# Kernel optimization log

Measured on AMD Instinct MI355X. Metric: run time of the kernel, lower is better.

Reference implementation:

```python
import jax, jax.numpy as jnp
import numpy as np

D = 512        # embed_dim
H = 2048       # expert hidden (4*D)
E = 8          # num_experts
TOPK = 2       # num_experts_per_tok


def setup_inputs() -> dict:
    key = jax.random.key(0)
    ks = jax.random.split(key, 5)
    s = 0.02
    x = jax.random.normal(ks[0], (4, 8192, D), dtype=jnp.float32)
    gate_w = jax.random.normal(ks[1], (D, E), dtype=jnp.float32) * s
    W1 = jax.random.normal(ks[2], (E, D, H), dtype=jnp.float32) * s
    W3 = jax.random.normal(ks[3], (E, D, H), dtype=jnp.float32) * s
    W2 = jax.random.normal(ks[4], (E, H, D), dtype=jnp.float32) * s
    return {"x": x, "gate_w": gate_w, "W1": W1, "W2": W2, "W3": W3}


def reference(x, gate_w, W1, W2, W3):
    B, S, _ = x.shape
    xt = x.reshape(-1, D)                      # [T, D]
    T = xt.shape[0]
    gate_logits = xt @ gate_w                  # [T, E]
    w, idx = jax.lax.top_k(gate_logits, TOPK)  # [T, k]
    w = jax.nn.softmax(w, axis=1).astype(xt.dtype)
    # combine weights: comb[t, e] = routing weight of expert e for token t (0 if unselected)
    comb = jnp.zeros((T, E), dtype=xt.dtype).at[jnp.arange(T)[:, None], idx].add(w)
    out = jnp.zeros_like(xt)
    for e in range(E):
        h = jax.nn.silu(xt @ W1[e]) * (xt @ W3[e])   # [T, H]
        out = out + (h @ W2[e]) * comb[:, e:e + 1]
    return out.reshape(B, S, D)
```

## Files before the change

### kernel.cpp

```cpp
#include <hip/hip_runtime.h>
#include <stdint.h>

#define D_DIM 512
#define H_DIM 2048
#define E_NUM 8
#define TOPK_N 2

typedef __attribute__((ext_vector_type(8))) short bf16x8;
typedef __attribute__((ext_vector_type(4))) float f32x4;

#define GLOAD_LDS16(gsrc, ldst)                                                     \
    __builtin_amdgcn_global_load_lds(                                               \
        (const __attribute__((address_space(1))) void*)(gsrc),                      \
        (__attribute__((address_space(3))) void*)(ldst), 16, 0, 0)

static __device__ __forceinline__ unsigned short f2bf(float f) {
    unsigned u = __float_as_uint(f);
    unsigned r = (u + 0x7fffu + ((u >> 16) & 1u)) >> 16;
    return (unsigned short)r;
}

__global__ void init_kernel(int* list_token, float* list_w, unsigned short* zrow, int cap) {
    int id = blockIdx.x * blockDim.x + threadIdx.x;
    if (id < cap) { list_token[id] = -1; list_w[id] = 0.f; }
    if (id < D_DIM) zrow[id] = 0;
}

__global__ void gwt_kernel(const float* __restrict__ gw, float* __restrict__ gwT) {
    int id = blockIdx.x * blockDim.x + threadIdx.x;
    int e = id >> 9, d = id & 511;
    gwT[id] = gw[d * E_NUM + e];
}

__global__ void gate_cvt_kernel(const float* __restrict__ x, const float* __restrict__ gwT,
                                unsigned short* __restrict__ xb,
                                int* __restrict__ ridx, float* __restrict__ rw, int T) {
    int wave = threadIdx.x >> 6;
    int lane = threadIdx.x & 63;
    int t = blockIdx.x * 4 + wave;
    if (t >= T) return;
    const float* xr = x + (size_t)t * D_DIM + lane * 8;
    float4 a = *(const float4*)xr;
    float4 b = *(const float4*)(xr + 4);
    union { unsigned short s[8]; uint4 v; } o;
    o.s[0] = f2bf(a.x); o.s[1] = f2bf(a.y); o.s[2] = f2bf(a.z); o.s[3] = f2bf(a.w);
    o.s[4] = f2bf(b.x); o.s[5] = f2bf(b.y); o.s[6] = f2bf(b.z); o.s[7] = f2bf(b.w);
    *(uint4*)(xb + (size_t)t * D_DIM + lane * 8) = o.v;
    float acc[8];
#pragma unroll
    for (int e = 0; e < 8; ++e) {
        const float* g = gwT + e * D_DIM + lane * 8;
        float4 g0 = *(const float4*)g;
        float4 g1 = *(const float4*)(g + 4);
        acc[e] = a.x * g0.x + a.y * g0.y + a.z * g0.z + a.w * g0.w
               + b.x * g1.x + b.y * g1.y + b.z * g1.z + b.w * g1.w;
    }
#pragma unroll
    for (int off = 32; off > 0; off >>= 1) {
#pragma unroll
        for (int e = 0; e < 8; ++e) acc[e] += __shfl_xor(acc[e], off, 64);
    }
    if (lane == 0) {
        int e0 = 0; float l0 = acc[0];
#pragma unroll
        for (int e = 1; e < 8; ++e) if (acc[e] > l0) { l0 = acc[e]; e0 = e; }
        int e1 = -1; float l1 = -1e30f;
#pragma unroll
        for (int e = 0; e < 8; ++e) if (e != e0 && acc[e] > l1) { l1 = acc[e]; e1 = e; }
        float w0 = 1.f / (1.f + expf(l1 - l0));
        ridx[t * 2] = e0; ridx[t * 2 + 1] = e1;
        rw[t * 2] = w0;  rw[t * 2 + 1] = 1.f - w0;
    }
}

__global__ void tconv_kernel(const float* __restrict__ in, unsigned short* __restrict__ out,
                             int R, int C) {
    __shared__ float tile[32][33];
    int e = blockIdx.z;
    const float* src = in + (size_t)e * R * C;
    unsigned short* dst = out + (size_t)e * R * C;
    int c = blockIdx.x * 32 + threadIdx.x;
#pragma unroll
    for (int i = 0; i < 4; ++i) {
        int r = blockIdx.y * 32 + threadIdx.y + i * 8;
        tile[threadIdx.y + i * 8][threadIdx.x] = src[(size_t)r * C + c];
    }
    __syncthreads();
    int r2 = blockIdx.y * 32 + threadIdx.x;
#pragma unroll
    for (int i = 0; i < 4; ++i) {
        int c2 = blockIdx.x * 32 + threadIdx.y + i * 8;
        dst[(size_t)c2 * R + r2] = f2bf(tile[threadIdx.x][threadIdx.y + i * 8]);
    }
}

__global__ void hist_kernel(const int* __restrict__ ridx, int* __restrict__ partial, int npairs) {
    __shared__ int cnt[E_NUM];
    if (threadIdx.x < E_NUM) cnt[threadIdx.x] = 0;
    __syncthreads();
    for (int i = blockIdx.x * blockDim.x + threadIdx.x; i < npairs; i += gridDim.x * blockDim.x)
        atomicAdd(&cnt[ridx[i]], 1);
    __syncthreads();
    if (threadIdx.x < E_NUM) partial[blockIdx.x * E_NUM + threadIdx.x] = cnt[threadIdx.x];
}

__global__ void scan_kernel(const int* __restrict__ partial, int* __restrict__ seg,
                            int* __restrict__ block_base) {
    __shared__ int sp[64 * E_NUM];
    __shared__ int segl[E_NUM + 1];
    int tid = threadIdx.x;
    if (tid < 64 * E_NUM) sp[tid] = partial[tid];
    __syncthreads();
    if (tid == 0) {
        int off = 0;
        for (int e = 0; e < E_NUM; ++e) {
            segl[e] = off;
            int c = 0;
            for (int b = 0; b < 64; ++b) c += sp[b * E_NUM + e];
            off += (c + 127) & ~127;
        }
        segl[E_NUM] = off;
    }
    __syncthreads();
    if (tid < E_NUM) {
        int run = segl[tid];
        for (int b = 0; b < 64; ++b) { block_base[b * E_NUM + tid] = run; run += sp[b * E_NUM + tid]; }
        seg[tid] = segl[tid];
        if (tid == 0) seg[E_NUM] = segl[E_NUM];
    }
}

__global__ void scatter_kernel(const int* __restrict__ ridx, const float* __restrict__ rw,
                               const int* __restrict__ block_base,
                               int* __restrict__ list_token, float* __restrict__ list_w, int npairs) {
    __shared__ int base[E_NUM];
    __shared__ int cnt[E_NUM];
    if (threadIdx.x < E_NUM) { base[threadIdx.x] = block_base[blockIdx.x * E_NUM + threadIdx.x]; cnt[threadIdx.x] = 0; }
    __syncthreads();
    for (int i = blockIdx.x * blockDim.x + threadIdx.x; i < npairs; i += gridDim.x * blockDim.x) {
        int e = ridx[i];
        int pos = base[e] + atomicAdd(&cnt[e], 1);
        list_token[pos] = i >> 1;
        list_w[pos] = rw[i];
    }
}

__global__ __launch_bounds__(256) void gemm1_kernel(
    const unsigned short* __restrict__ xb,
    const unsigned short* __restrict__ w1t,
    const unsigned short* __restrict__ w3t,
    const unsigned short* __restrict__ zrow,
    const int* __restrict__ list_token,
    const int* __restrict__ seg,
    unsigned short* __restrict__ hbuf,
    int chunk_base, int MT, int MG) {
    __shared__ short As[128 * 64];
    __shared__ short Bs[128 * 64];

    int bfl = blockIdx.x;
    int xcd = bfl & 7;
    int idx = bfl >> 3;
    int mlocal = idx % MG;
    int yt = idx / MG;
    int mt = mlocal * 8 + xcd;
    if (mt >= MT) return;

    int tid = threadIdx.x;
    int w = tid >> 6, l = tid & 63;
    int m0 = mt * 128;
    int slot0 = chunk_base + m0;
    int n0 = yt * 64;

    int e = 0;
#pragma unroll
    for (int i = 0; i < E_NUM - 1; ++i) if (slot0 >= seg[i + 1]) e = i + 1;
    const unsigned short* b1 = w1t + ((size_t)e * H_DIM + n0) * D_DIM;
    const unsigned short* b3 = w3t + ((size_t)e * H_DIM + n0) * D_DIM;

    int lr8 = l >> 3, p = l & 7;
    const unsigned short* aptr[4];
    const unsigned short* bptr[4];
#pragma unroll
    for (int q = 0; q < 4; ++q) {
        int row = (q * 4 + w) * 8 + lr8;
        int c = p ^ (row & 7);
        int tok = list_token[slot0 + row];
        aptr[q] = (tok >= 0 ? xb + (size_t)tok * D_DIM : zrow) + c * 8;
        bptr[q] = (row < 64 ? b1 + (size_t)row * D_DIM
                            : b3 + (size_t)(row - 64) * D_DIM) + c * 8;
    }

    int wm = (w & 1) * 64;
    int wn = (w >> 1) * 32;
    int lrr = l & 15;
    int lk = (l >> 4) * 8;

    f32x4 acc1[4][2] = {};
    f32x4 acc3[4][2] = {};

    for (int k0 = 0; k0 < D_DIM; k0 += 64) {
#pragma unroll
        for (int q = 0; q < 4; ++q) {
            GLOAD_LDS16(aptr[q] + k0, &As[(q * 4 + w) * 512]);
            GLOAD_LDS16(bptr[q] + k0, &Bs[(q * 4 + w) * 512]);
        }
        __syncthreads();
#pragma unroll
        for (int ks = 0; ks < 64; ks += 32) {
            int cblk = (ks + lk) >> 3;
            bf16x8 af[4], b1f[2], b3f[2];
#pragma unroll
            for (int i = 0; i < 4; ++i) {
                int row = wm + i * 16 + lrr;
                af[i] = *(const bf16x8*)&As[row * 64 + ((cblk ^ (row & 7)) << 3)];
            }
#pragma unroll
            for (int j = 0; j < 2; ++j) {
                int r1 = wn + j * 16 + lrr;
                b1f[j] = *(const bf16x8*)&Bs[r1 * 64 + ((cblk ^ (r1 & 7)) << 3)];
                int r3 = 64 + wn + j * 16 + lrr;
                b3f[j] = *(const bf16x8*)&Bs[r3 * 64 + ((cblk ^ (r3 & 7)) << 3)];
            }
#pragma unroll
            for (int i = 0; i < 4; ++i)
#pragma unroll
                for (int j = 0; j < 2; ++j) {
                    acc1[i][j] = __builtin_amdgcn_mfma_f32_16x16x32_bf16(af[i], b1f[j], acc1[i][j], 0, 0, 0);
                    acc3[i][j] = __builtin_amdgcn_mfma_f32_16x16x32_bf16(af[i], b3f[j], acc3[i][j], 0, 0, 0);
                }
        }
        __syncthreads();
    }

    int lrow0 = (l >> 4) * 4, lcol = l & 15;
#pragma unroll
    for (int i = 0; i < 4; ++i)
#pragma unroll
        for (int j = 0; j < 2; ++j)
#pragma unroll
            for (int r = 0; r < 4; ++r) {
                int row = wm + i * 16 + lrow0 + r;
                int col = wn + j * 16 + lcol;
                float v1 = acc1[i][j][r];
                float v3 = acc3[i][j][r];
                float h = v1 / (1.f + expf(-v1)) * v3;
                hbuf[(size_t)(m0 + row) * H_DIM + n0 + col] = f2bf(h);
            }
}

__global__ __launch_bounds__(256) void gemm2_kernel(
    const unsigned short* __restrict__ hbuf,
    const unsigned short* __restrict__ w2t,
    const int* __restrict__ list_token,
    const float* __restrict__ list_w,
    const int* __restrict__ seg,
    float* __restrict__ out,
    int chunk_base, int MT) {
    __shared__ short As[128 * 64];
    __shared__ short Bs[128 * 64];
    __shared__ int ltok[128];
    __shared__ float lw[128];

    int bfl = blockIdx.x;
    int xcd = bfl & 7;
    int idx = bfl >> 3;
    int yt = idx & 3;
    int mlocal = idx >> 2;
    int mt = mlocal * 8 + xcd;
    if (mt >= MT) return;

    int tid = threadIdx.x;
    int w = tid >> 6, l = tid & 63;
    int m0 = mt * 128;
    int slot0 = chunk_base + m0;
    int n0 = yt * 128;

    if (tid < 128) { ltok[tid] = list_token[slot0 + tid]; lw[tid] = list_w[slot0 + tid]; }

    int e = 0;
#pragma unroll
    for (int i = 0; i < E_NUM - 1; ++i) if (slot0 >= seg[i + 1]) e = i + 1;
    const unsigned short* b2 = w2t + ((size_t)e * D_DIM + n0) * H_DIM;

    int lr8 = l >> 3, p = l & 7;
    const unsigned short* aptr[4];
    const unsigned short* bptr[4];
#pragma unroll
    for (int q = 0; q < 4; ++q) {
        int row = (q * 4 + w) * 8 + lr8;
        int c = p ^ (row & 7);
        aptr[q] = hbuf + (size_t)(m0 + row) * H_DIM + c * 8;
        bptr[q] = b2 + (size_t)row * H_DIM + c * 8;
    }

    int wm = (w & 1) * 64;
    int wn = (w >> 1) * 64;
    int lrr = l & 15;
    int lk = (l >> 4) * 8;

    f32x4 acc[4][4] = {};

    for (int k0 = 0; k0 < H_DIM; k0 += 64) {
#pragma unroll
        for (int q = 0; q < 4; ++q) {
            GLOAD_LDS16(aptr[q] + k0, &As[(q * 4 + w) * 512]);
            GLOAD_LDS16(bptr[q] + k0, &Bs[(q * 4 + w) * 512]);
        }
        __syncthreads();
#pragma unroll
        for (int ks = 0; ks < 64; ks += 32) {
            int cblk = (ks + lk) >> 3;
            bf16x8 af[4], bf[4];
#pragma unroll
            for (int i = 0; i < 4; ++i) {
                int row = wm + i * 16 + lrr;
                af[i] = *(const bf16x8*)&As[row * 64 + ((cblk ^ (row & 7)) << 3)];
            }
#pragma unroll
            for (int j = 0; j < 4; ++j) {
                int row = wn + j * 16 + lrr;
                bf[j] = *(const bf16x8*)&Bs[row * 64 + ((cblk ^ (row & 7)) << 3)];
            }
#pragma unroll
            for (int i = 0; i < 4; ++i)
#pragma unroll
                for (int j = 0; j < 4; ++j)
                    acc[i][j] = __builtin_amdgcn_mfma_f32_16x16x32_bf16(af[i], bf[j], acc[i][j], 0, 0, 0);
        }
        __syncthreads();
    }

    int lrow0 = (l >> 4) * 4, lcol = l & 15;
#pragma unroll
    for (int i = 0; i < 4; ++i)
#pragma unroll
        for (int j = 0; j < 4; ++j)
#pragma unroll
            for (int r = 0; r < 4; ++r) {
                int row = wm + i * 16 + lrow0 + r;
                int col = wn + j * 16 + lcol;
                int tok = ltok[row];
                if (tok >= 0)
                    atomicAdd(&out[(size_t)tok * D_DIM + n0 + col], acc[i][j][r] * lw[row]);
            }
}

extern "C" void kernel_launch(void* const* d_in, const int* in_sizes, int n_in,
                              void* d_out, int out_size, void* d_ws, size_t ws_size,
                              hipStream_t stream) {
    const float* x  = (const float*)d_in[0];
    const float* gw = (const float*)d_in[1];
    const float* W1 = (const float*)d_in[2];
    const float* W2 = (const float*)d_in[3];
    const float* W3 = (const float*)d_in[4];
    float* out = (float*)d_out;

    int T = in_sizes[0] / D_DIM;
    int npairs = T * TOPK_N;
    const int CAP = npairs + E_NUM * 128;
    const int NCHUNK = 4;
    int chunk_slots = CAP / NCHUNK;
    int MT = chunk_slots / 128;
    int MG = (MT + 7) / 8;

    char* p = (char*)d_ws;
    size_t off = 0;
    auto take = [&](size_t bytes) {
        char* r = p + off;
        off = (off + bytes + 255) & ~(size_t)255;
        return r;
    };
    int* seg           = (int*)take((E_NUM + 1) * 4);
    int* partial       = (int*)take(64 * E_NUM * 4);
    int* block_base    = (int*)take(64 * E_NUM * 4);
    int* list_token    = (int*)take((size_t)CAP * 4);
    float* list_w      = (float*)take((size_t)CAP * 4);
    int* ridx          = (int*)take((size_t)npairs * 4);
    float* rw          = (float*)take((size_t)npairs * 4);
    float* gwT         = (float*)take((size_t)E_NUM * D_DIM * 4);
    unsigned short* zrow = (unsigned short*)take((size_t)D_DIM * 2);
    unsigned short* xb  = (unsigned short*)take((size_t)T * D_DIM * 2);
    unsigned short* w1t = (unsigned short*)take((size_t)E_NUM * D_DIM * H_DIM * 2);
    unsigned short* w3t = (unsigned short*)take((size_t)E_NUM * D_DIM * H_DIM * 2);
    unsigned short* w2t = (unsigned short*)take((size_t)E_NUM * D_DIM * H_DIM * 2);
    unsigned short* hbuf = (unsigned short*)take((size_t)chunk_slots * H_DIM * 2);
    (void)ws_size;

    hipMemsetAsync(d_out, 0, (size_t)out_size * sizeof(float), stream);

    init_kernel<<<(CAP + 255) / 256, 256, 0, stream>>>(list_token, list_w, zrow, CAP);
    gwt_kernel<<<(E_NUM * D_DIM) / 256, 256, 0, stream>>>(gw, gwT);

    gate_cvt_kernel<<<T / 4, 256, 0, stream>>>(x, gwT, xb, ridx, rw, T);

    dim3 tb(32, 8);
    tconv_kernel<<<dim3(H_DIM / 32, D_DIM / 32, E_NUM), tb, 0, stream>>>(W1, w1t, D_DIM, H_DIM);
    tconv_kernel<<<dim3(H_DIM / 32, D_DIM / 32, E_NUM), tb, 0, stream>>>(W3, w3t, D_DIM, H_DIM);
    tconv_kernel<<<dim3(D_DIM / 32, H_DIM / 32, E_NUM), tb, 0, stream>>>(W2, w2t, H_DIM, D_DIM);

    hist_kernel<<<64, 256, 0, stream>>>(ridx, partial, npairs);
    scan_kernel<<<1, 512, 0, stream>>>(partial, seg, block_base);
    scatter_kernel<<<64, 256, 0, stream>>>(ridx, rw, block_base, list_token, list_w, npairs);

    int g1_grid = 8 * MG * (H_DIM / 64);
    int g2_grid = 8 * MG * (D_DIM / 128);
    for (int c = 0; c < NCHUNK; ++c) {
        int cb = c * chunk_slots;
        gemm1_kernel<<<g1_grid, 256, 0, stream>>>(
            xb, w1t, w3t, zrow, list_token, seg, hbuf, cb, MT, MG);
        gemm2_kernel<<<g2_grid, 256, 0, stream>>>(
            hbuf, w2t, list_token, list_w, seg, out, cb, MT);
    }
}
```

Before: 1.020 ms.

## Double-buffer LDS tiles in both expert GEMMs and use fewer, larger chunks

Both expert GEMM kernels now use two LDS buffers, so the global-to-LDS load of the next K tile is issued while MFMAs run on the current one. The MFMA blocks are wrapped in s_setprio, and SiLU uses the fast __expf. When the workspace is large enough, tokens are processed in two chunks instead of four, which means fewer launches and a larger hbuf. The gemm2 epilogue reads token ids and weights straight from global memory instead of staging them in LDS. The cost is double the LDS per block, which may reduce occupancy.

Result: faster. 917.0 us (-10.1%).

```diff
diff --git a/kernel.cpp b/kernel.cpp
--- a/kernel.cpp
+++ b/kernel.cpp
@@ -154,8 +154,8 @@
     const int* __restrict__ seg,
     unsigned short* __restrict__ hbuf,
     int chunk_base, int MT, int MG) {
-    __shared__ short As[128 * 64];
-    __shared__ short Bs[128 * 64];
+    __shared__ short As[2][128 * 64];
+    __shared__ short Bs[2][128 * 64];
 
     int bfl = blockIdx.x;
     int xcd = bfl & 7;
@@ -198,39 +198,58 @@
     f32x4 acc1[4][2] = {};
     f32x4 acc3[4][2] = {};
 
-    for (int k0 = 0; k0 < D_DIM; k0 += 64) {
-#pragma unroll
-        for (int q = 0; q < 4; ++q) {
-            GLOAD_LDS16(aptr[q] + k0, &As[(q * 4 + w) * 512]);
-            GLOAD_LDS16(bptr[q] + k0, &Bs[(q * 4 + w) * 512]);
-        }
+#define G1_STAGE(K0, BUF)                                                           \
+    {                                                                               \
+        _Pragma("unroll")                                                           \
+        for (int q = 0; q < 4; ++q) {                                               \
+            GLOAD_LDS16(aptr[q] + (K0), &As[BUF][(q * 4 + w) * 512]);               \
+            GLOAD_LDS16(bptr[q] + (K0), &Bs[BUF][(q * 4 + w) * 512]);               \
+        }                                                                           \
+    }
+
+#define G1_COMPUTE(BUF)                                                             \
+    {                                                                               \
+        _Pragma("unroll")                                                           \
+        for (int ks = 0; ks < 64; ks += 32) {                                       \
+            int cblk = (ks + lk) >> 3;                                              \
+            bf16x8 af[4], b1f[2], b3f[2];                                           \
+            _Pragma("unroll")                                                       \
+            for (int i = 0; i < 4; ++i) {                                           \
+                int row = wm + i * 16 + lrr;                                        \
+                af[i] = *(const bf16x8*)&As[BUF][row * 64 + ((cblk ^ (row & 7)) << 3)]; \
+            }                                                                       \
+            _Pragma("unroll")                                                       \
+            for (int j = 0; j < 2; ++j) {                                           \
+                int r1 = wn + j * 16 + lrr;                                         \
+                b1f[j] = *(const bf16x8*)&Bs[BUF][r1 * 64 + ((cblk ^ (r1 & 7)) << 3)]; \
+                int r3 = 64 + wn + j * 16 + lrr;                                    \
+                b3f[j] = *(const bf16x8*)&Bs[BUF][r3 * 64 + ((cblk ^ (r3 & 7)) << 3)]; \
+            }                                                                       \
+            __builtin_amdgcn_s_setprio(1);                                          \
+            _Pragma("unroll")                                                       \
+            for (int i = 0; i < 4; ++i)                                             \
+                _Pragma("unroll")                                                   \
+                for (int j = 0; j < 2; ++j) {                                       \
+                    acc1[i][j] = __builtin_amdgcn_mfma_f32_16x16x32_bf16(af[i], b1f[j], acc1[i][j], 0, 0, 0); \
+                    acc3[i][j] = __builtin_amdgcn_mfma_f32_16x16x32_bf16(af[i], b3f[j], acc3[i][j], 0, 0, 0); \
+                }                                                                   \
+            __builtin_amdgcn_s_setprio(0);                                          \
+        }                                                                           \
+    }
+
+    G1_STAGE(0, 0);
+    __syncthreads();
+#pragma unroll
+    for (int t = 0; t < 8; t += 2) {
+        G1_STAGE((t + 1) * 64, 1);
+        G1_COMPUTE(0);
         __syncthreads();
-#pragma unroll
-        for (int ks = 0; ks < 64; ks += 32) {
-            int cblk = (ks + lk) >> 3;
-            bf16x8 af[4], b1f[2], b3f[2];
-#pragma unroll
-            for (int i = 0; i < 4; ++i) {
-                int row = wm + i * 16 + lrr;
-                af[i] = *(const bf16x8*)&As[row * 64 + ((cblk ^ (row & 7)) << 3)];
-            }
-#pragma unroll
-            for (int j = 0; j < 2; ++j) {
-                int r1 = wn + j * 16 + lrr;
-                b1f[j] = *(const bf16x8*)&Bs[r1 * 64 + ((cblk ^ (r1 & 7)) << 3)];
-                int r3 = 64 + wn + j * 16 + lrr;
-                b3f[j] = *(const bf16x8*)&Bs[r3 * 64 + ((cblk ^ (r3 & 7)) << 3)];
-            }
-#pragma unroll
-            for (int i = 0; i < 4; ++i)
-#pragma unroll
-                for (int j = 0; j < 2; ++j) {
-                    acc1[i][j] = __builtin_amdgcn_mfma_f32_16x16x32_bf16(af[i], b1f[j], acc1[i][j], 0, 0, 0);
-                    acc3[i][j] = __builtin_amdgcn_mfma_f32_16x16x32_bf16(af[i], b3f[j], acc3[i][j], 0, 0, 0);
-                }
-        }
+        if (t + 2 < 8) G1_STAGE((t + 2) * 64, 0);
+        G1_COMPUTE(1);
         __syncthreads();
     }
+#undef G1_STAGE
+#undef G1_COMPUTE
 
     int lrow0 = (l >> 4) * 4, lcol = l & 15;
 #pragma unroll
@@ -243,7 +262,7 @@
                 int col = wn + j * 16 + lcol;
                 float v1 = acc1[i][j][r];
                 float v3 = acc3[i][j][r];
-                float h = v1 / (1.f + expf(-v1)) * v3;
+                float h = v1 / (1.f + __expf(-v1)) * v3;
                 hbuf[(size_t)(m0 + row) * H_DIM + n0 + col] = f2bf(h);
             }
 }
@@ -256,10 +275,8 @@
     const int* __restrict__ seg,
     float* __restrict__ out,
     int chunk_base, int MT) {
-    __shared__ short As[128 * 64];
-    __shared__ short Bs[128 * 64];
-    __shared__ int ltok[128];
-    __shared__ float lw[128];
+    __shared__ short As[2][128 * 64];
+    __shared__ short Bs[2][128 * 64];
 
     int bfl = blockIdx.x;
     int xcd = bfl & 7;
@@ -275,8 +292,6 @@
     int slot0 = chunk_base + m0;
     int n0 = yt * 128;
 
-    if (tid < 128) { ltok[tid] = list_token[slot0 + tid]; lw[tid] = list_w[slot0 + tid]; }
-
     int e = 0;
 #pragma unroll
     for (int i = 0; i < E_NUM - 1; ++i) if (slot0 >= seg[i + 1]) e = i + 1;
@@ -300,49 +315,69 @@
 
     f32x4 acc[4][4] = {};
 
-    for (int k0 = 0; k0 < H_DIM; k0 += 64) {
-#pragma unroll
-        for (int q = 0; q < 4; ++q) {
-            GLOAD_LDS16(aptr[q] + k0, &As[(q * 4 + w) * 512]);
-            GLOAD_LDS16(bptr[q] + k0, &Bs[(q * 4 + w) * 512]);
+#define G2_STAGE(K0, BUF)                                                           \
+    {                                                                               \
+        _Pragma("unroll")                                                           \
+        for (int q = 0; q < 4; ++q) {                                               \
+            GLOAD_LDS16(aptr[q] + (K0), &As[BUF][(q * 4 + w) * 512]);               \
+            GLOAD_LDS16(bptr[q] + (K0), &Bs[BUF][(q * 4 + w) * 512]);               \
+        }                                                                           \
+    }
+
+#define G2_COMPUTE(BUF)                                                             \
+    {                                                                               \
+        _Pragma("unroll")                                                           \
+        for (int ks = 0; ks < 64; ks += 32) {                                       \
+            int cblk = (ks + lk) >> 3;                                              \
+            bf16x8 af[4], bf[4];                                                    \
+            _Pragma("unroll")                                                       \
+            for (int i = 0; i < 4; ++i) {                                           \
+                int row = wm + i * 16 + lrr;                                        \
+                af[i] = *(const bf16x8*)&As[BUF][row * 64 + ((cblk ^ (row & 7)) << 3)]; \
+            }                                                                       \
+            _Pragma("unroll")                                                       \
+            for (int j = 0; j < 4; ++j) {                                           \
+                int row = wn + j * 16 + lrr;                                        \
+                bf[j] = *(const bf16x8*)&Bs[BUF][row * 64 + ((cblk ^ (row & 7)) << 3)]; \
+            }                                                                       \
+            __builtin_amdgcn_s_setprio(1);                                          \
+            _Pragma("unroll")                                                       \
+            for (int i = 0; i < 4; ++i)                                             \
+                _Pragma("unroll")                                                   \
+                for (int j = 0; j < 4; ++j)                                         \
+                    acc[i][j] = __builtin_amdgcn_mfma_f32_16x16x32_bf16(af[i], bf[j], acc[i][j], 0, 0, 0); \
+            __builtin_amdgcn_s_setprio(0);                                          \
+        }                                                                           \
+    }
+
+    G2_STAGE(0, 0);
+    __syncthreads();
+    for (int t = 0; t < 32; t += 2) {
+        G2_STAGE((t + 1) * 64, 1);
+        G2_COMPUTE(0);
+        __syncthreads();
+        if (t + 2 < 32) G2_STAGE((t + 2) * 64, 0);
+        G2_COMPUTE(1);
+        __syncthreads();
+    }
+#undef G2_STAGE
+#undef G2_COMPUTE
+
+    int lrow0 = (l >> 4) * 4, lcol = l & 15;
+#pragma unroll
+    for (int i = 0; i < 4; ++i)
+#pragma unroll
+        for (int r = 0; r < 4; ++r) {
+            int row = wm + i * 16 + lrow0 + r;
+            int tok = list_token[slot0 + row];
+            if (tok < 0) continue;
+            float wgt = list_w[slot0 + row];
+#pragma unroll
+            for (int j = 0; j < 4; ++j) {
+                int col = wn + j * 16 + lcol;
+                atomicAdd(&out[(size_t)tok * D_DIM + n0 + col], acc[i][j][r] * wgt);
+            }
         }
-        __syncthreads();
-#pragma unroll
-        for (int ks = 0; ks < 64; ks += 32) {
-            int cblk = (ks + lk) >> 3;
-            bf16x8 af[4], bf[4];
-#pragma unroll
-            for (int i = 0; i < 4; ++i) {
-                int row = wm + i * 16 + lrr;
-                af[i] = *(const bf16x8*)&As[row * 64 + ((cblk ^ (row & 7)) << 3)];
-            }
-#pragma unroll
-            for (int j = 0; j < 4; ++j) {
-                int row = wn + j * 16 + lrr;
-                bf[j] = *(const bf16x8*)&Bs[row * 64 + ((cblk ^ (row & 7)) << 3)];
-            }
-#pragma unroll
-            for (int i = 0; i < 4; ++i)
-#pragma unroll
-                for (int j = 0; j < 4; ++j)
-                    acc[i][j] = __builtin_amdgcn_mfma_f32_16x16x32_bf16(af[i], bf[j], acc[i][j], 0, 0, 0);
-        }
-        __syncthreads();
-    }
-
-    int lrow0 = (l >> 4) * 4, lcol = l & 15;
-#pragma unroll
-    for (int i = 0; i < 4; ++i)
-#pragma unroll
-        for (int j = 0; j < 4; ++j)
-#pragma unroll
-            for (int r = 0; r < 4; ++r) {
-                int row = wm + i * 16 + lrow0 + r;
-                int col = wn + j * 16 + lcol;
-                int tok = ltok[row];
-                if (tok >= 0)
-                    atomicAdd(&out[(size_t)tok * D_DIM + n0 + col], acc[i][j][r] * lw[row]);
-            }
 }
 
 extern "C" void kernel_launch(void* const* d_in, const int* in_sizes, int n_in,
@@ -358,10 +393,6 @@
     int T = in_sizes[0] / D_DIM;
     int npairs = T * TOPK_N;
     const int CAP = npairs + E_NUM * 128;
-    const int NCHUNK = 4;
-    int chunk_slots = CAP / NCHUNK;
-    int MT = chunk_slots / 128;
-    int MG = (MT + 7) / 8;
 
     char* p = (char*)d_ws;
     size_t off = 0;
@@ -383,8 +414,13 @@
     unsigned short* w1t = (unsigned short*)take((size_t)E_NUM * D_DIM * H_DIM * 2);
     unsigned short* w3t = (unsigned short*)take((size_t)E_NUM * D_DIM * H_DIM * 2);
     unsigned short* w2t = (unsigned short*)take((size_t)E_NUM * D_DIM * H_DIM * 2);
+
+    size_t hbuf2_bytes = (size_t)(CAP / 2) * H_DIM * 2;
+    int NCHUNK = (ws_size >= off + hbuf2_bytes + 4096) ? 2 : 4;
+    int chunk_slots = CAP / NCHUNK;
+    int MT = chunk_slots / 128;
+    int MG = (MT + 7) / 8;
     unsigned short* hbuf = (unsigned short*)take((size_t)chunk_slots * H_DIM * 2);
-    (void)ws_size;
 
     hipMemsetAsync(d_out, 0, (size_t)out_size * sizeof(float), stream);
 
```
